# Performance work log

Measured on AMD Instinct MI355X. Metric: run time of the kernel, lower is better.

## Reference

```python
import jax, jax.numpy as jnp
import numpy as np

N_AUTHOR = 50000
N_PAPER = 50000
D_IN = 128      # input feature dim == hidden_channels so both layers share weight shapes
HID = 128
OUT = 32
N_LAYERS = 2
N_EDGES = 800000
NEG_SLOPE = 0.01  # F.leaky_relu default


def setup_inputs() -> dict:
    key = jax.random.key(0)
    ks = jax.random.split(key, 10)
    return {
        "x_author": jax.random.normal(ks[0], (N_AUTHOR, D_IN), jnp.float32),
        "x_paper": jax.random.normal(ks[1], (N_PAPER, D_IN), jnp.float32),
        # edge_index[0] = source node ids, edge_index[1] = destination node ids
        "edge_writes": jax.random.randint(ks[2], (2, N_EDGES), 0, N_PAPER, jnp.int32),      # author -> paper
        "edge_written_by": jax.random.randint(ks[3], (2, N_EDGES), 0, N_AUTHOR, jnp.int32),  # paper  -> author
        "edge_cites": jax.random.randint(ks[4], (2, N_EDGES), 0, N_PAPER, jnp.int32),        # paper  -> paper
        # SAGEConv params, stacked [layer, relation, in, out]; relation order:
        # 0: writes (a->p), 1: written_by (p->a), 2: cites (p->p)
        "Wl": jax.random.normal(ks[5], (N_LAYERS, 3, D_IN, HID), jnp.float32) * 0.05,  # lin_l (messages, has bias)
        "bl": jnp.zeros((N_LAYERS, 3, HID), jnp.float32),
        "Wr": jax.random.normal(ks[6], (N_LAYERS, 3, D_IN, HID), jnp.float32) * 0.05,  # lin_r (root, no bias)
        "lin_W": jax.random.normal(ks[7], (HID, OUT), jnp.float32) * 0.05,
        "lin_b": jnp.zeros((OUT,), jnp.float32),
    }


def _mean_aggr(x_src, edge, n_dst):
    # mean of source features over incoming edges per destination node; 0 for isolated nodes
    src, dst = edge[0], edge[1]
    s = jax.ops.segment_sum(x_src[src], dst, num_segments=n_dst)           # [n_dst, d]
    cnt = jax.ops.segment_sum(jnp.ones((dst.shape[0],), x_src.dtype), dst, num_segments=n_dst)
    return s / jnp.maximum(cnt, 1.0)[:, None]


def _sage(x_src, x_dst, edge, W_l, b_l, W_r):
    # PyG SAGEConv (mean aggr): lin_l(mean_j x_src[j]) + lin_r(x_dst)
    return _mean_aggr(x_src, edge, x_dst.shape[0]) @ W_l + b_l + x_dst @ W_r


def reference(x_author, x_paper, edge_writes, edge_written_by, edge_cites,
              Wl, bl, Wr, lin_W, lin_b):
    a, p = x_author, x_paper
    for l in range(N_LAYERS):
        # HeteroConv default aggr='sum' over edge types sharing a dst node type
        p_new = (_sage(a, p, edge_writes, Wl[l, 0], bl[l, 0], Wr[l, 0])
                 + _sage(p, p, edge_cites, Wl[l, 2], bl[l, 2], Wr[l, 2]))
        a_new = _sage(p, a, edge_written_by, Wl[l, 1], bl[l, 1], Wr[l, 1])
        a = jax.nn.leaky_relu(a_new, NEG_SLOPE)
        p = jax.nn.leaky_relu(p_new, NEG_SLOPE)
    return a @ lin_W + lin_b  # [N_AUTHOR, OUT]
```

## Files before the change

### kernel.cpp

```cpp
#include <hip/hip_runtime.h>

#define NA 50000
#define NP 50000
#define NE 800000
#define D 128
#define OUTD 32
#define NSEG 150000
#define DD (D * D)
#define NCH 196
#define NBK 588
#define CHE 4096
#define ZROW 50000

typedef float f32x4 __attribute__((ext_vector_type(4)));
typedef short s16x8 __attribute__((ext_vector_type(8)));

__device__ __forceinline__ ushort f2b(float f) {
    uint x = __float_as_uint(f);
    x += ((x >> 16) & 1u) + 0x7fffu;
    return (ushort)(x >> 16);
}


#define CVT_BLOCKS 12500
#define PREP_BLOCKS 466
#define HIST_BLOCKS NBK

__global__ __launch_bounds__(256) void front(
    const float* __restrict__ xa, const float* __restrict__ xp,
    ushort* __restrict__ oa, ushort* __restrict__ op,
    const float* __restrict__ Wl, const float* __restrict__ Wr,
    const float* __restrict__ linW, const float* __restrict__ bl,
    ushort* __restrict__ wt, float* __restrict__ bsum_p,
    ushort* __restrict__ p1b,
    const int* __restrict__ dw, const int* __restrict__ dc, const int* __restrict__ dwb,
    int* __restrict__ Hglob)
{
    __shared__ int hist[NCH];
    int b = blockIdx.x, t = threadIdx.x;
    if (b < CVT_BLOCKS) {
        int i = b * 256 + t;
        const int per = NA * D / 4;
        const float* src; ushort* dst; int li;
        if (i < per) { src = xa; dst = oa; li = i; }
        else { src = xp; dst = op; li = i - per; }
        float4 v = *(const float4*)&src[(size_t)li * 4];
        ushort4 o;
        o.x = f2b(v.x); o.y = f2b(v.y); o.z = f2b(v.z); o.w = f2b(v.w);
        *(ushort4*)&dst[(size_t)li * 4] = o;
    } else if (b < CVT_BLOCKS + PREP_BLOCKS) {
        int b2 = b - CVT_BLOCKS;
        if (b2 < 448) {
            int job = b2 >> 6;
            int idx = (b2 & 63) * 256 + t;
            int n = idx >> 7, k = idx & 127;
            const float* src;
            float add = 0.f;
            switch (job) {
                case 0: src = Wl + 0 * DD; break;
                case 1: src = Wl + 2 * DD; break;
                case 2: src = Wr + 0 * DD; add = Wr[2 * DD + k * D + n]; break;
                case 3: src = Wl + 1 * DD; break;
                case 4: src = Wr + 1 * DD; break;
                case 5: src = Wl + 4 * DD; break;
                default: src = Wr + 4 * DD; break;
            }
            wt[(size_t)job * DD + idx] = f2b(src[k * D + n] + add);
        } else if (b2 < 464) {
            int idx = (b2 - 448) * 256 + t;
            int n = idx >> 7, k = idx & 127;
            wt[(size_t)7 * DD + idx] = f2b(linW[k * OUTD + n]);
        } else if (b2 == 464) {
            if (t < D) bsum_p[t] = bl[t] + bl[2 * D + t];
        } else {
            if (t < 64)       ((uint*)(oa + (size_t)ZROW * D))[t] = 0;
            else if (t < 128) ((uint*)(op + (size_t)ZROW * D))[t - 64] = 0;
            else if (t < 192) ((uint*)(p1b + (size_t)ZROW * D))[t - 128] = 0;
        }
    } else {
        int hb = b - CVT_BLOCKS - PREP_BLOCKS;
        int r = hb / NCH, c = hb % NCH;
        const int* dp = (r == 0) ? dw : ((r == 1) ? dc : dwb);
        for (int i = t; i < NCH; i += 256) hist[i] = 0;
        __syncthreads();
        int base = c * CHE;
#pragma unroll
        for (int i = 0; i < 16; ++i) {
            int e = base + i * 256 + t;
            if (e < NE) atomicAdd(&hist[dp[e] >> 8], 1);
        }
        __syncthreads();
        for (int dg = t; dg < NCH; dg += 256)
            Hglob[(r * NCH + dg) * NCH + c] = hist[dg];
    }
}


__global__ __launch_bounds__(64) void scan_chunks(
    const int* __restrict__ Hglob, int* __restrict__ OFF, int* __restrict__ T)
{
    int gd = blockIdx.x, t = threadIdx.x;
    int carry = 0;
#pragma unroll
    for (int rnd = 0; rnd < 4; ++rnd) {
        int idx = rnd * 64 + t;
        int v = (idx < NCH) ? Hglob[gd * NCH + idx] : 0;
        int x = v;
#pragma unroll
        for (int off = 1; off < 64; off <<= 1) {
            int y = __shfl_up(x, off, 64);
            if (t >= off) x += y;
        }
        if (idx < NCH) OFF[gd * NCH + idx] = carry + x - v;
        carry += __shfl(x, 63, 64);
    }
    if (t == 0) T[gd] = carry;
}


__global__ __launch_bounds__(64) void scan_buckets(
    const int* __restrict__ T, int* __restrict__ B)
{
    int t = threadIdx.x, carry = 0;
#pragma unroll
    for (int rnd = 0; rnd < 10; ++rnd) {
        int idx = rnd * 64 + t;
        int v = (idx < NBK) ? T[idx] : 0;
        int x = v;
#pragma unroll
        for (int off = 1; off < 64; off <<= 1) {
            int y = __shfl_up(x, off, 64);
            if (t >= off) x += y;
        }
        if (idx < NBK) B[idx] = carry + x - v;
        carry += __shfl(x, 63, 64);
    }
}


__global__ __launch_bounds__(256) void bucket_scatter(
    const int* __restrict__ sw, const int* __restrict__ dw,
    const int* __restrict__ sc_, const int* __restrict__ dc,
    const int* __restrict__ swb, const int* __restrict__ dwb,
    const int* __restrict__ B, const int* __restrict__ OFF,
    uint* __restrict__ bucketed)
{
    __shared__ int lbase[NCH];
    __shared__ int cnt2[NCH];
    int b = blockIdx.x, t = threadIdx.x;
    int r = b / NCH, c = b % NCH;
    const int* sp = (r == 0) ? sw : ((r == 1) ? sc_ : swb);
    const int* dp = (r == 0) ? dw : ((r == 1) ? dc : dwb);
    for (int i = t; i < NCH; i += 256) {
        int gd = r * NCH + i;
        lbase[i] = B[gd] + OFF[gd * NCH + c];
        cnt2[i] = 0;
    }
    __syncthreads();
    int base = c * CHE;
#pragma unroll
    for (int i = 0; i < 16; ++i) {
        int e = base + i * 256 + t;
        if (e < NE) {
            int d = dp[e], s = sp[e];
            int dg = d >> 8;
            int rk = atomicAdd(&cnt2[dg], 1);
            bucketed[lbase[dg] + rk] = ((uint)d << 16) | (uint)s;
        }
    }
}


__global__ __launch_bounds__(256) void bucket_sort(
    const uint* __restrict__ bucketed, const int* __restrict__ B,
    const int* __restrict__ T, ushort* __restrict__ csr16,
    int* __restrict__ rowptr)
{
    __shared__ int h[256], bb[256], c3[256];
    int gd = blockIdx.x, t = threadIdx.x;
    int r = gd / NCH, hb = gd % NCH;
    int beg = B[gd], n = T[gd];
    h[t] = 0; c3[t] = 0;
    __syncthreads();
    for (int i = t; i < n; i += 256)
        atomicAdd(&h[(bucketed[beg + i] >> 16) & 255], 1);
    __syncthreads();
    if (t < 64) {
        int carry = 0;
#pragma unroll
        for (int rnd = 0; rnd < 4; ++rnd) {
            int idx = rnd * 64 + t;
            int v = h[idx], x = v;
#pragma unroll
            for (int off = 1; off < 64; off <<= 1) {
                int y = __shfl_up(x, off, 64);
                if (t >= off) x += y;
            }
            bb[idx] = carry + x - v;
            carry += __shfl(x, 63, 64);
        }
    }
    __syncthreads();
    {
        int dst = hb * 256 + t;
        if (dst < 50000) rowptr[r * 50000 + dst] = beg + bb[t];
    }
    for (int i = t; i < n; i += 256) {
        uint rec = bucketed[beg + i];
        int low = (rec >> 16) & 255;
        int rk = atomicAdd(&c3[low], 1);
        csr16[beg + bb[low] + rk] = (ushort)(rec & 0xffffu);
    }
    if (gd == NBK - 1 && t == 0) rowptr[NSEG] = 3 * NE;
}


#define DOT2(a, u, m) asm("v_dot2_f32_bf16 %0, %1, %2, %0" : "+v"(a) : "v"(u), "v"(m))

__device__ __forceinline__ void gather_node(
    const ushort* __restrict__ x, const ushort* __restrict__ bk, int n,
    int l, int g, int c, ushort* __restrict__ outp)
{
    float acc[8];
#pragma unroll
    for (int k = 0; k < 8; ++k) acc[k] = 0.f;
    const uint mlo = 0x00003f80u;
    const uint mhi = 0x3f800000u;
    const uint cb = (uint)c * 16;

    for (int base = 0; base < n; base += 64) {
        int rem = n - base;
        int m = rem > 64 ? 64 : rem;
        int idx = (l < m) ? (int)bk[base + l] : ZROW;
        int mceil = (m + 3) & ~3;
#pragma unroll 2
        for (int j = 0; j < mceil; j += 4) {
            int row = __shfl(idx, j + g, 64);
            uint4 u = *(const uint4*)((const char*)x + (((uint)row << 8) + cb));
            DOT2(acc[0], u.x, mlo); DOT2(acc[1], u.x, mhi);
            DOT2(acc[2], u.y, mlo); DOT2(acc[3], u.y, mhi);
            DOT2(acc[4], u.z, mlo); DOT2(acc[5], u.z, mhi);
            DOT2(acc[6], u.w, mlo); DOT2(acc[7], u.w, mhi);
        }
    }
#pragma unroll
    for (int k = 0; k < 8; ++k) {
        acc[k] += __shfl_xor(acc[k], 16, 64);
        acc[k] += __shfl_xor(acc[k], 32, 64);
    }
    if (g == 0) {
        float scl = (n > 0) ? 1.0f / (float)n : 0.f;
        uint4 o;
        o.x = (uint)f2b(acc[0] * scl) | ((uint)f2b(acc[1] * scl) << 16);
        o.y = (uint)f2b(acc[2] * scl) | ((uint)f2b(acc[3] * scl) << 16);
        o.z = (uint)f2b(acc[4] * scl) | ((uint)f2b(acc[5] * scl) << 16);
        o.w = (uint)f2b(acc[6] * scl) | ((uint)f2b(acc[7] * scl) << 16);
        *(uint4*)&outp[c * 8] = o;
    }
}

__global__ __launch_bounds__(256) void gather3(
    const ushort* __restrict__ xa, const ushort* __restrict__ xp,
    const int* __restrict__ rowptr, const ushort* __restrict__ csr16,
    ushort* __restrict__ agg3)
{
    int wid = (blockIdx.x * 256 + threadIdx.x) >> 6;
    if (wid >= NSEG) return;
    const ushort* x = (wid < 50000) ? xa : xp;
    int l = threadIdx.x & 63;
    int beg = __builtin_amdgcn_readfirstlane(rowptr[wid]);
    int end = __builtin_amdgcn_readfirstlane(rowptr[wid + 1]);
    gather_node(x, csr16 + beg, end - beg, l, l >> 4, l & 15,
                agg3 + (size_t)wid * D);
}

__global__ __launch_bounds__(256) void gather_l1(
    const ushort* __restrict__ x, const int* __restrict__ rowptr,
    const ushort* __restrict__ csr16, ushort* __restrict__ out)
{
    int wid = (blockIdx.x * 256 + threadIdx.x) >> 6;
    if (wid >= NA) return;
    int l = threadIdx.x & 63;
    int beg = __builtin_amdgcn_readfirstlane(rowptr[100000 + wid]);
    int end = __builtin_amdgcn_readfirstlane(rowptr[100000 + wid + 1]);
    gather_node(x, csr16 + beg, end - beg, l, l >> 4, l & 15,
                out + (size_t)wid * D);
}


#define LDA 136

__device__ __forceinline__ void gemm_core(
    ushort* As, f32x4 (&acc)[2][4],
    const ushort* __restrict__ A0, const ushort* __restrict__ WT0,
    const ushort* __restrict__ A1, const ushort* __restrict__ WT1,
    const ushort* __restrict__ A2, const ushort* __restrict__ WT2,
    int nseg, int brow, int M)
{
    const int t = threadIdx.x;
    const int w = t >> 6;
    const int l = t & 63;
    const int wr = w >> 1, wc = w & 1;
    const int l15 = l & 15, l4 = l >> 4;

    for (int s = 0; s < nseg; ++s) {
        const ushort* A = (s == 0) ? A0 : ((s == 1) ? A1 : A2);
        const ushort* WT = (s == 0) ? WT0 : ((s == 1) ? WT1 : WT2);

        if (s) __syncthreads();
#pragma unroll
        for (int it = 0; it < 4; ++it) {
            int f = it * 256 + t;
            int row = f >> 4, cc = f & 15;
            int grow = brow + row;
            float4 v = make_float4(0.f, 0.f, 0.f, 0.f);
            if (grow < M) v = *(const float4*)&A[(size_t)grow * D + cc * 8];
            *(float4*)&As[row * LDA + cc * 8] = v;
        }
        s16x8 Bf[4][4];
#pragma unroll
        for (int ni = 0; ni < 4; ++ni)
#pragma unroll
            for (int ks = 0; ks < 4; ++ks)
                Bf[ni][ks] = *(const s16x8*)&WT[(size_t)(wc * 64 + ni * 16 + l15) * D + ks * 32 + l4 * 8];
        __syncthreads();

#pragma unroll
        for (int ks = 0; ks < 4; ++ks) {
            s16x8 af[2];
#pragma unroll
            for (int mi = 0; mi < 2; ++mi)
                af[mi] = *(const s16x8*)&As[(wr * 32 + mi * 16 + l15) * LDA + ks * 32 + l4 * 8];
#pragma unroll
            for (int mi = 0; mi < 2; ++mi)
#pragma unroll
                for (int ni = 0; ni < 4; ++ni)
                    acc[mi][ni] = __builtin_amdgcn_mfma_f32_16x16x32_bf16(
                        af[mi], Bf[ni][ks], acc[mi][ni], 0, 0, 0);
        }
    }
}

__global__ __launch_bounds__(256) void gemm_pair(
    const ushort* __restrict__ agg3, const ushort* __restrict__ xb_p,
    const ushort* __restrict__ xb_a, const ushort* __restrict__ wt,
    const float* __restrict__ bsum_p, const float* __restrict__ bl,
    ushort* __restrict__ p1b, ushort* __restrict__ a1b)
{
    __shared__ ushort As[64 * LDA];
    const int t = threadIdx.x;
    const int w = t >> 6;
    const int l = t & 63;
    const int wr = w >> 1, wc = w & 1;
    const int l15 = l & 15, l4 = l >> 4;

    f32x4 acc[2][4];
#pragma unroll
    for (int i = 0; i < 2; ++i)
#pragma unroll
        for (int j = 0; j < 4; ++j) acc[i][j] = (f32x4){0.f, 0.f, 0.f, 0.f};

    bool isP = blockIdx.x < 782;
    int bIdx = isP ? blockIdx.x : blockIdx.x - 782;
    int brow = bIdx * 64;
    const float* bias;
    ushort* C;
    if (isP) {
        gemm_core(As, acc, agg3, wt + 0 * DD, agg3 + (size_t)50000 * D, wt + 1 * DD,
                  xb_p, wt + 2 * DD, 3, brow, NP);
        bias = bsum_p; C = p1b;
    } else {
        gemm_core(As, acc, agg3 + (size_t)100000 * D, wt + 3 * DD, xb_a, wt + 4 * DD,
                  nullptr, nullptr, 2, brow, NA);
        bias = bl + 1 * D; C = a1b;
    }

#pragma unroll
    for (int mi = 0; mi < 2; ++mi) {
#pragma unroll
        for (int ni = 0; ni < 4; ++ni) {
            int col = wc * 64 + ni * 16 + l15;
            float bb = bias[col];
#pragma unroll
            for (int r = 0; r < 4; ++r) {
                int grow = brow + wr * 32 + mi * 16 + l4 * 4 + r;
                if (grow >= 50000) continue;
                float v = acc[mi][ni][r] + bb;
                v = v > 0.f ? v : 0.01f * v;
                C[(size_t)grow * D + col] = f2b(v);
            }
        }
    }
}

__global__ __launch_bounds__(256) void gemm_final(
    const ushort* __restrict__ A0, const ushort* __restrict__ WT0,
    const ushort* __restrict__ A1, const ushort* __restrict__ WT1,
    const float* __restrict__ bias,
    const ushort* __restrict__ linWT, const float* __restrict__ linb,
    float* __restrict__ fout, int M)
{
    __shared__ ushort As[64 * LDA];
    const int t = threadIdx.x;
    const int w = t >> 6;
    const int l = t & 63;
    const int wr = w >> 1, wc = w & 1;
    const int l15 = l & 15, l4 = l >> 4;
    const int brow = blockIdx.x * 64;

    f32x4 acc[2][4];
#pragma unroll
    for (int i = 0; i < 2; ++i)
#pragma unroll
        for (int j = 0; j < 4; ++j) acc[i][j] = (f32x4){0.f, 0.f, 0.f, 0.f};

    gemm_core(As, acc, A0, WT0, A1, WT1, nullptr, nullptr, 2, brow, M);

    __syncthreads();
#pragma unroll
    for (int mi = 0; mi < 2; ++mi) {
#pragma unroll
        for (int ni = 0; ni < 4; ++ni) {
            int col = wc * 64 + ni * 16 + l15;
            float bb = bias[col];
#pragma unroll
            for (int r = 0; r < 4; ++r) {
                int row = wr * 32 + mi * 16 + l4 * 4 + r;
                float v = acc[mi][ni][r] + bb;
                v = v > 0.f ? v : 0.01f * v;
                As[row * LDA + col] = f2b(v);
            }
        }
    }
    __syncthreads();
    f32x4 a2c[2];
    a2c[0] = (f32x4){0.f, 0.f, 0.f, 0.f};
    a2c[1] = (f32x4){0.f, 0.f, 0.f, 0.f};
#pragma unroll
    for (int ks = 0; ks < 4; ++ks) {
        s16x8 af = *(const s16x8*)&As[(w * 16 + l15) * LDA + ks * 32 + l4 * 8];
#pragma unroll
        for (int ni = 0; ni < 2; ++ni) {
            s16x8 bf = *(const s16x8*)&linWT[(size_t)(ni * 16 + l15) * D + ks * 32 + l4 * 8];
            a2c[ni] = __builtin_amdgcn_mfma_f32_16x16x32_bf16(af, bf, a2c[ni], 0, 0, 0);
        }
    }
#pragma unroll
    for (int ni = 0; ni < 2; ++ni) {
        int col = ni * 16 + l15;
        float bb = linb[col];
#pragma unroll
        for (int r = 0; r < 4; ++r) {
            int grow = brow + w * 16 + l4 * 4 + r;
            if (grow < M) fout[(size_t)grow * OUTD + col] = a2c[ni][r] + bb;
        }
    }
}


extern "C" void kernel_launch(void* const* d_in, const int* in_sizes, int n_in,
                              void* d_out, int out_size, void* d_ws, size_t ws_size,
                              hipStream_t stream)
{
    const float* x_author = (const float*)d_in[0];
    const float* x_paper  = (const float*)d_in[1];
    const int*   e_w      = (const int*)d_in[2];
    const int*   e_wb     = (const int*)d_in[3];
    const int*   e_c      = (const int*)d_in[4];
    const float* Wl       = (const float*)d_in[5];
    const float* bl       = (const float*)d_in[6];
    const float* Wr       = (const float*)d_in[7];
    const float* linW     = (const float*)d_in[8];
    const float* linb     = (const float*)d_in[9];
    float* out = (float*)d_out;

    int* ib = (int*)d_ws;
    int* Hglob  = ib;
    int* OFF    = ib + 115248;
    int* T      = ib + 230496;
    int* B      = ib + 231084;
    int* rowptr = ib + 231680;
    uint* bucketed = (uint*)(ib + 381696);
    ushort* csr16  = (ushort*)(ib + 2781696);
    float* bsum_p  = (float*)(ib + 3981696);
    ushort* ub = (ushort*)(ib + 3981824);
    const size_t R1 = 50001 * (size_t)D;
    ushort* wt   = ub;
    ushort* xb_a = ub + 131072;
    ushort* xb_p = xb_a + R1;
    ushort* agg3 = xb_p + R1;
    ushort* p1b  = agg3 + (size_t)NSEG * D;
    ushort* a1b  = p1b + R1;
    ushort* g2b  = agg3;

    front<<<CVT_BLOCKS + PREP_BLOCKS + HIST_BLOCKS, 256, 0, stream>>>(
        x_author, x_paper, xb_a, xb_p,
        Wl, Wr, linW, bl, wt, bsum_p, p1b,
        e_w + NE, e_c + NE, e_wb + NE, Hglob);

    scan_chunks<<<NBK, 64, 0, stream>>>(Hglob, OFF, T);
    scan_buckets<<<1, 64, 0, stream>>>(T, B);

    bucket_scatter<<<NBK, 256, 0, stream>>>(
        e_w, e_w + NE, e_c, e_c + NE, e_wb, e_wb + NE, B, OFF, bucketed);

    bucket_sort<<<NBK, 256, 0, stream>>>(bucketed, B, T, csr16, rowptr);

    gather3<<<NSEG * 64 / 256, 256, 0, stream>>>(xb_a, xb_p, rowptr, csr16, agg3);

    gemm_pair<<<1564, 256, 0, stream>>>(agg3, xb_p, xb_a, wt, bsum_p, bl, p1b, a1b);

    gather_l1<<<NA * 64 / 256, 256, 0, stream>>>(p1b, rowptr, csr16, g2b);

    gemm_final<<<(NA + 63) / 64, 256, 0, stream>>>(
        g2b, wt + 5 * DD, a1b, wt + 6 * DD, bl + 4 * D, wt + 7 * DD, linb, out, NA);
}
```

Baseline: 247.4 us.

## Process four destination nodes per wavefront in gather kernels

Each wavefront now gathers neighbours for four destination nodes at once, interleaving their row loads so more independent memory requests are in flight per wave. Launch grids shrink by four accordingly, and lists longer than 64 entries fall back to a per-node tail loop. The trade-off is lanes wasted padding to the longest of the four lists, plus higher register use from the wider accumulators, which may lower occupancy.

Measured after the change: 255.3 us. +3.2%, slower.

```diff
diff --git a/kernel.cpp b/kernel.cpp
--- a/kernel.cpp
+++ b/kernel.cpp
@@ -217,45 +217,101 @@
 
 #define DOT2(a, u, m) asm("v_dot2_f32_bf16 %0, %1, %2, %0" : "+v"(a) : "v"(u), "v"(m))
 
-__device__ __forceinline__ void gather_node(
-    const ushort* __restrict__ x, const ushort* __restrict__ bk, int n,
-    int l, int g, int c, ushort* __restrict__ outp)
-{
-    float acc[8];
-#pragma unroll
-    for (int k = 0; k < 8; ++k) acc[k] = 0.f;
+__device__ __forceinline__ void gather4_core(
+    const ushort* __restrict__ x0, const ushort* __restrict__ x1, int thr,
+    const int* __restrict__ rowptr, int wid0,
+    const ushort* __restrict__ csr16, ushort* __restrict__ out)
+{
+    const int l = threadIdx.x & 63;
+    const int g = l >> 4, c = l & 15;
+    const uint cb = (uint)c * 16;
     const uint mlo = 0x00003f80u;
     const uint mhi = 0x3f800000u;
-    const uint cb = (uint)c * 16;
-
-    for (int base = 0; base < n; base += 64) {
-        int rem = n - base;
-        int m = rem > 64 ? 64 : rem;
-        int idx = (l < m) ? (int)bk[base + l] : ZROW;
-        int mceil = (m + 3) & ~3;
-#pragma unroll 2
-        for (int j = 0; j < mceil; j += 4) {
-            int row = __shfl(idx, j + g, 64);
-            uint4 u = *(const uint4*)((const char*)x + (((uint)row << 8) + cb));
-            DOT2(acc[0], u.x, mlo); DOT2(acc[1], u.x, mhi);
-            DOT2(acc[2], u.y, mlo); DOT2(acc[3], u.y, mhi);
-            DOT2(acc[4], u.z, mlo); DOT2(acc[5], u.z, mhi);
-            DOT2(acc[6], u.w, mlo); DOT2(acc[7], u.w, mhi);
-        }
-    }
-#pragma unroll
-    for (int k = 0; k < 8; ++k) {
-        acc[k] += __shfl_xor(acc[k], 16, 64);
-        acc[k] += __shfl_xor(acc[k], 32, 64);
-    }
-    if (g == 0) {
-        float scl = (n > 0) ? 1.0f / (float)n : 0.f;
-        uint4 o;
-        o.x = (uint)f2b(acc[0] * scl) | ((uint)f2b(acc[1] * scl) << 16);
-        o.y = (uint)f2b(acc[2] * scl) | ((uint)f2b(acc[3] * scl) << 16);
-        o.z = (uint)f2b(acc[4] * scl) | ((uint)f2b(acc[5] * scl) << 16);
-        o.w = (uint)f2b(acc[6] * scl) | ((uint)f2b(acc[7] * scl) << 16);
-        *(uint4*)&outp[c * 8] = o;
+
+    int rp = rowptr[wid0 + (l > 4 ? 4 : l)];
+    int beg[4], n[4], mc[4];
+#pragma unroll
+    for (int k = 0; k < 4; ++k) {
+        beg[k] = __builtin_amdgcn_readfirstlane(__shfl(rp, k, 64));
+        int e = __builtin_amdgcn_readfirstlane(__shfl(rp, k + 1, 64));
+        n[k] = e - beg[k];
+        int m = n[k] > 64 ? 64 : n[k];
+        mc[k] = (m + 3) & ~3;
+    }
+    int maxmc = mc[0];
+    maxmc = mc[1] > maxmc ? mc[1] : maxmc;
+    maxmc = mc[2] > maxmc ? mc[2] : maxmc;
+    maxmc = mc[3] > maxmc ? mc[3] : maxmc;
+
+    const ushort* xs[4];
+#pragma unroll
+    for (int k = 0; k < 4; ++k) xs[k] = (wid0 + k < thr) ? x0 : x1;
+
+    int idx[4];
+#pragma unroll
+    for (int k = 0; k < 4; ++k) {
+        int m = n[k] > 64 ? 64 : n[k];
+        idx[k] = (l < m) ? (int)csr16[beg[k] + l] : ZROW;
+    }
+
+    float acc[4][8];
+#pragma unroll
+    for (int k = 0; k < 4; ++k)
+#pragma unroll
+        for (int i = 0; i < 8; ++i) acc[k][i] = 0.f;
+
+    for (int j = 0; j < maxmc; j += 4) {
+        uint4 u[4];
+#pragma unroll
+        for (int k = 0; k < 4; ++k) {
+            int row = __shfl(idx[k], j + g, 64);
+            u[k] = *(const uint4*)((const char*)xs[k] + (((uint)row << 8) + cb));
+        }
+#pragma unroll
+        for (int k = 0; k < 4; ++k) {
+            DOT2(acc[k][0], u[k].x, mlo); DOT2(acc[k][1], u[k].x, mhi);
+            DOT2(acc[k][2], u[k].y, mlo); DOT2(acc[k][3], u[k].y, mhi);
+            DOT2(acc[k][4], u[k].z, mlo); DOT2(acc[k][5], u[k].z, mhi);
+            DOT2(acc[k][6], u[k].w, mlo); DOT2(acc[k][7], u[k].w, mhi);
+        }
+    }
+
+#pragma unroll
+    for (int k = 0; k < 4; ++k) {
+        if (n[k] > 64) {
+            for (int base = 64; base < n[k]; base += 64) {
+                int rem = n[k] - base;
+                int m = rem > 64 ? 64 : rem;
+                int id2 = (l < m) ? (int)csr16[beg[k] + base + l] : ZROW;
+                int mc2 = (m + 3) & ~3;
+                for (int j = 0; j < mc2; j += 4) {
+                    int row = __shfl(id2, j + g, 64);
+                    uint4 u = *(const uint4*)((const char*)xs[k] + (((uint)row << 8) + cb));
+                    DOT2(acc[k][0], u.x, mlo); DOT2(acc[k][1], u.x, mhi);
+                    DOT2(acc[k][2], u.y, mlo); DOT2(acc[k][3], u.y, mhi);
+                    DOT2(acc[k][4], u.z, mlo); DOT2(acc[k][5], u.z, mhi);
+                    DOT2(acc[k][6], u.w, mlo); DOT2(acc[k][7], u.w, mhi);
+                }
+            }
+        }
+    }
+
+#pragma unroll
+    for (int k = 0; k < 4; ++k) {
+#pragma unroll
+        for (int i = 0; i < 8; ++i) {
+            acc[k][i] += __shfl_xor(acc[k][i], 16, 64);
+            acc[k][i] += __shfl_xor(acc[k][i], 32, 64);
+        }
+        if (g == 0) {
+            float scl = (n[k] > 0) ? 1.0f / (float)n[k] : 0.f;
+            uint4 o;
+            o.x = (uint)f2b(acc[k][0] * scl) | ((uint)f2b(acc[k][1] * scl) << 16);
+            o.y = (uint)f2b(acc[k][2] * scl) | ((uint)f2b(acc[k][3] * scl) << 16);
+            o.z = (uint)f2b(acc[k][4] * scl) | ((uint)f2b(acc[k][5] * scl) << 16);
+            o.w = (uint)f2b(acc[k][6] * scl) | ((uint)f2b(acc[k][7] * scl) << 16);
+            *(uint4*)&out[(size_t)(wid0 + k) * D + c * 8] = o;
+        }
     }
 }
 
@@ -264,27 +320,20 @@
     const int* __restrict__ rowptr, const ushort* __restrict__ csr16,
     ushort* __restrict__ agg3)
 {
-    int wid = (blockIdx.x * 256 + threadIdx.x) >> 6;
-    if (wid >= NSEG) return;
-    const ushort* x = (wid < 50000) ? xa : xp;
-    int l = threadIdx.x & 63;
-    int beg = __builtin_amdgcn_readfirstlane(rowptr[wid]);
-    int end = __builtin_amdgcn_readfirstlane(rowptr[wid + 1]);
-    gather_node(x, csr16 + beg, end - beg, l, l >> 4, l & 15,
-                agg3 + (size_t)wid * D);
+    int wv = (blockIdx.x * 256 + threadIdx.x) >> 6;
+    int wid0 = wv * 4;
+    if (wid0 >= NSEG) return;
+    gather4_core(xa, xp, 50000, rowptr, wid0, csr16, agg3);
 }
 
 __global__ __launch_bounds__(256) void gather_l1(
     const ushort* __restrict__ x, const int* __restrict__ rowptr,
     const ushort* __restrict__ csr16, ushort* __restrict__ out)
 {
-    int wid = (blockIdx.x * 256 + threadIdx.x) >> 6;
-    if (wid >= NA) return;
-    int l = threadIdx.x & 63;
-    int beg = __builtin_amdgcn_readfirstlane(rowptr[100000 + wid]);
-    int end = __builtin_amdgcn_readfirstlane(rowptr[100000 + wid + 1]);
-    gather_node(x, csr16 + beg, end - beg, l, l >> 4, l & 15,
-                out + (size_t)wid * D);
+    int wv = (blockIdx.x * 256 + threadIdx.x) >> 6;
+    int wid0 = wv * 4;
+    if (wid0 >= NA) return;
+    gather4_core(x, x, NSEG, rowptr + 100000, wid0, csr16, out);
 }
 
 
@@ -506,11 +555,11 @@
 
     bucket_sort<<<NBK, 256, 0, stream>>>(bucketed, B, T, csr16, rowptr);
 
-    gather3<<<NSEG * 64 / 256, 256, 0, stream>>>(xb_a, xb_p, rowptr, csr16, agg3);
+    gather3<<<NSEG / 4 / 4, 256, 0, stream>>>(xb_a, xb_p, rowptr, csr16, agg3);
 
     gemm_pair<<<1564, 256, 0, stream>>>(agg3, xb_p, xb_a, wt, bsum_p, bl, p1b, a1b);
 
-    gather_l1<<<NA * 64 / 256, 256, 0, stream>>>(p1b, rowptr, csr16, g2b);
+    gather_l1<<<NA / 4 / 4, 256, 0, stream>>>(p1b, rowptr, csr16, g2b);
 
     gemm_final<<<(NA + 63) / 64, 256, 0, stream>>>(
         g2b, wt + 5 * DD, a1b, wt + 6 * DD, bl + 4 * D, wt + 7 * DD, linb, out, NA);
```

## Fuse neighbor mean-aggregation gathers into the SAGE GEMM kernels via LDS staging

Applied to the files above, without the earlier changes.

The separate gather kernels, which wrote bf16 aggregates to global memory, are removed. The GEMM blocks now gather their own 64 destination rows straight into shared memory and run MFMA on them. This drops the global round trip for agg3/g2b and two kernel launches. Weight fragments are now loaded per k-step instead of being preloaded into registers. Occupancy falls from 2344 gather blocks to 1564/782 fused blocks, and the GEMM blocks now stall on irregular gathers, so latency hiding may suffer.

After: 294.9 us. 1.19x slower.

```diff
diff --git a/kernel.cpp b/kernel.cpp
--- a/kernel.cpp
+++ b/kernel.cpp
@@ -215,144 +215,110 @@
 }
 
 
+#define LDA 136
 #define DOT2(a, u, m) asm("v_dot2_f32_bf16 %0, %1, %2, %0" : "+v"(a) : "v"(u), "v"(m))
 
-__device__ __forceinline__ void gather_node(
-    const ushort* __restrict__ x, const ushort* __restrict__ bk, int n,
-    int l, int g, int c, ushort* __restrict__ outp)
-{
-    float acc[8];
-#pragma unroll
-    for (int k = 0; k < 8; ++k) acc[k] = 0.f;
+__device__ __forceinline__ void gather_seg(
+    const ushort* __restrict__ x, const int* __restrict__ rowptr,
+    int gnbase, const ushort* __restrict__ csr16, ushort* As)
+{
+    const int t = threadIdx.x;
+    const int w = t >> 6, l = t & 63;
+    const int g = l >> 4, c = l & 15;
+    const uint cb = (uint)c * 16;
     const uint mlo = 0x00003f80u;
     const uint mhi = 0x3f800000u;
-    const uint cb = (uint)c * 16;
-
-    for (int base = 0; base < n; base += 64) {
-        int rem = n - base;
-        int m = rem > 64 ? 64 : rem;
-        int idx = (l < m) ? (int)bk[base + l] : ZROW;
-        int mceil = (m + 3) & ~3;
 #pragma unroll 2
-        for (int j = 0; j < mceil; j += 4) {
-            int row = __shfl(idx, j + g, 64);
-            uint4 u = *(const uint4*)((const char*)x + (((uint)row << 8) + cb));
-            DOT2(acc[0], u.x, mlo); DOT2(acc[1], u.x, mhi);
-            DOT2(acc[2], u.y, mlo); DOT2(acc[3], u.y, mhi);
-            DOT2(acc[4], u.z, mlo); DOT2(acc[5], u.z, mhi);
-            DOT2(acc[6], u.w, mlo); DOT2(acc[7], u.w, mhi);
-        }
-    }
-#pragma unroll
-    for (int k = 0; k < 8; ++k) {
-        acc[k] += __shfl_xor(acc[k], 16, 64);
-        acc[k] += __shfl_xor(acc[k], 32, 64);
-    }
-    if (g == 0) {
-        float scl = (n > 0) ? 1.0f / (float)n : 0.f;
-        uint4 o;
-        o.x = (uint)f2b(acc[0] * scl) | ((uint)f2b(acc[1] * scl) << 16);
-        o.y = (uint)f2b(acc[2] * scl) | ((uint)f2b(acc[3] * scl) << 16);
-        o.z = (uint)f2b(acc[4] * scl) | ((uint)f2b(acc[5] * scl) << 16);
-        o.w = (uint)f2b(acc[6] * scl) | ((uint)f2b(acc[7] * scl) << 16);
-        *(uint4*)&outp[c * 8] = o;
-    }
-}
-
-__global__ __launch_bounds__(256) void gather3(
-    const ushort* __restrict__ xa, const ushort* __restrict__ xp,
+    for (int i = 0; i < 16; ++i) {
+        int nl = w * 16 + i;
+        int gn = gnbase + nl;
+        gn = gn > NSEG - 1 ? NSEG - 1 : gn;
+        int beg = __builtin_amdgcn_readfirstlane(rowptr[gn]);
+        int end = __builtin_amdgcn_readfirstlane(rowptr[gn + 1]);
+        int n = end - beg;
+        float acc[8];
+#pragma unroll
+        for (int k2 = 0; k2 < 8; ++k2) acc[k2] = 0.f;
+        for (int base = 0; base < n; base += 64) {
+            int rem = n - base;
+            int m = rem > 64 ? 64 : rem;
+            int idx = (l < m) ? (int)csr16[beg + base + l] : ZROW;
+            int mceil = (m + 3) & ~3;
+#pragma unroll 2
+            for (int j = 0; j < mceil; j += 4) {
+                int row = __shfl(idx, j + g, 64);
+                uint4 u = *(const uint4*)((const char*)x + (((uint)row << 8) + cb));
+                DOT2(acc[0], u.x, mlo); DOT2(acc[1], u.x, mhi);
+                DOT2(acc[2], u.y, mlo); DOT2(acc[3], u.y, mhi);
+                DOT2(acc[4], u.z, mlo); DOT2(acc[5], u.z, mhi);
+                DOT2(acc[6], u.w, mlo); DOT2(acc[7], u.w, mhi);
+            }
+        }
+#pragma unroll
+        for (int k2 = 0; k2 < 8; ++k2) {
+            acc[k2] += __shfl_xor(acc[k2], 16, 64);
+            acc[k2] += __shfl_xor(acc[k2], 32, 64);
+        }
+        if (g == 0) {
+            float scl = (n > 0) ? 1.0f / (float)n : 0.f;
+            uint4 o;
+            o.x = (uint)f2b(acc[0] * scl) | ((uint)f2b(acc[1] * scl) << 16);
+            o.y = (uint)f2b(acc[2] * scl) | ((uint)f2b(acc[3] * scl) << 16);
+            o.z = (uint)f2b(acc[4] * scl) | ((uint)f2b(acc[5] * scl) << 16);
+            o.w = (uint)f2b(acc[6] * scl) | ((uint)f2b(acc[7] * scl) << 16);
+            *(uint4*)&As[nl * LDA + c * 8] = o;
+        }
+    }
+}
+
+__device__ __forceinline__ void stage_direct(
+    const ushort* __restrict__ A, int brow, int M, ushort* As)
+{
+    const int t = threadIdx.x;
+#pragma unroll
+    for (int it = 0; it < 4; ++it) {
+        int f = it * 256 + t;
+        int row = f >> 4, cc = f & 15;
+        int grow = brow + row;
+        float4 v = make_float4(0.f, 0.f, 0.f, 0.f);
+        if (grow < M) v = *(const float4*)&A[(size_t)grow * D + cc * 8];
+        *(float4*)&As[row * LDA + cc * 8] = v;
+    }
+}
+
+__device__ __forceinline__ void mfma_seg(
+    const ushort* __restrict__ As, const ushort* __restrict__ WT,
+    f32x4 (&acc)[2][4])
+{
+    const int t = threadIdx.x, w = t >> 6, l = t & 63;
+    const int wr = w >> 1, wc = w & 1, l15 = l & 15, l4 = l >> 4;
+#pragma unroll
+    for (int ks = 0; ks < 4; ++ks) {
+        s16x8 af[2];
+#pragma unroll
+        for (int mi = 0; mi < 2; ++mi)
+            af[mi] = *(const s16x8*)&As[(wr * 32 + mi * 16 + l15) * LDA + ks * 32 + l4 * 8];
+#pragma unroll
+        for (int ni = 0; ni < 4; ++ni) {
+            s16x8 bf = *(const s16x8*)&WT[(size_t)(wc * 64 + ni * 16 + l15) * D + ks * 32 + l4 * 8];
+#pragma unroll
+            for (int mi = 0; mi < 2; ++mi)
+                acc[mi][ni] = __builtin_amdgcn_mfma_f32_16x16x32_bf16(af[mi], bf, acc[mi][ni], 0, 0, 0);
+        }
+    }
+}
+
+__global__ __launch_bounds__(256) void fused_pair(
+    const ushort* __restrict__ xb_a, const ushort* __restrict__ xb_p,
     const int* __restrict__ rowptr, const ushort* __restrict__ csr16,
-    ushort* __restrict__ agg3)
-{
-    int wid = (blockIdx.x * 256 + threadIdx.x) >> 6;
-    if (wid >= NSEG) return;
-    const ushort* x = (wid < 50000) ? xa : xp;
-    int l = threadIdx.x & 63;
-    int beg = __builtin_amdgcn_readfirstlane(rowptr[wid]);
-    int end = __builtin_amdgcn_readfirstlane(rowptr[wid + 1]);
-    gather_node(x, csr16 + beg, end - beg, l, l >> 4, l & 15,
-                agg3 + (size_t)wid * D);
-}
-
-__global__ __launch_bounds__(256) void gather_l1(
-    const ushort* __restrict__ x, const int* __restrict__ rowptr,
-    const ushort* __restrict__ csr16, ushort* __restrict__ out)
-{
-    int wid = (blockIdx.x * 256 + threadIdx.x) >> 6;
-    if (wid >= NA) return;
-    int l = threadIdx.x & 63;
-    int beg = __builtin_amdgcn_readfirstlane(rowptr[100000 + wid]);
-    int end = __builtin_amdgcn_readfirstlane(rowptr[100000 + wid + 1]);
-    gather_node(x, csr16 + beg, end - beg, l, l >> 4, l & 15,
-                out + (size_t)wid * D);
-}
-
-
-#define LDA 136
-
-__device__ __forceinline__ void gemm_core(
-    ushort* As, f32x4 (&acc)[2][4],
-    const ushort* __restrict__ A0, const ushort* __restrict__ WT0,
-    const ushort* __restrict__ A1, const ushort* __restrict__ WT1,
-    const ushort* __restrict__ A2, const ushort* __restrict__ WT2,
-    int nseg, int brow, int M)
-{
-    const int t = threadIdx.x;
-    const int w = t >> 6;
-    const int l = t & 63;
-    const int wr = w >> 1, wc = w & 1;
-    const int l15 = l & 15, l4 = l >> 4;
-
-    for (int s = 0; s < nseg; ++s) {
-        const ushort* A = (s == 0) ? A0 : ((s == 1) ? A1 : A2);
-        const ushort* WT = (s == 0) ? WT0 : ((s == 1) ? WT1 : WT2);
-
-        if (s) __syncthreads();
-#pragma unroll
-        for (int it = 0; it < 4; ++it) {
-            int f = it * 256 + t;
-            int row = f >> 4, cc = f & 15;
-            int grow = brow + row;
-            float4 v = make_float4(0.f, 0.f, 0.f, 0.f);
-            if (grow < M) v = *(const float4*)&A[(size_t)grow * D + cc * 8];
-            *(float4*)&As[row * LDA + cc * 8] = v;
-        }
-        s16x8 Bf[4][4];
-#pragma unroll
-        for (int ni = 0; ni < 4; ++ni)
-#pragma unroll
-            for (int ks = 0; ks < 4; ++ks)
-                Bf[ni][ks] = *(const s16x8*)&WT[(size_t)(wc * 64 + ni * 16 + l15) * D + ks * 32 + l4 * 8];
-        __syncthreads();
-
-#pragma unroll
-        for (int ks = 0; ks < 4; ++ks) {
-            s16x8 af[2];
-#pragma unroll
-            for (int mi = 0; mi < 2; ++mi)
-                af[mi] = *(const s16x8*)&As[(wr * 32 + mi * 16 + l15) * LDA + ks * 32 + l4 * 8];
-#pragma unroll
-            for (int mi = 0; mi < 2; ++mi)
-#pragma unroll
-                for (int ni = 0; ni < 4; ++ni)
-                    acc[mi][ni] = __builtin_amdgcn_mfma_f32_16x16x32_bf16(
-                        af[mi], Bf[ni][ks], acc[mi][ni], 0, 0, 0);
-        }
-    }
-}
-
-__global__ __launch_bounds__(256) void gemm_pair(
-    const ushort* __restrict__ agg3, const ushort* __restrict__ xb_p,
-    const ushort* __restrict__ xb_a, const ushort* __restrict__ wt,
-    const float* __restrict__ bsum_p, const float* __restrict__ bl,
+    const ushort* __restrict__ wt, const float* __restrict__ bsum_p,
+    const float* __restrict__ bl,
     ushort* __restrict__ p1b, ushort* __restrict__ a1b)
 {
     __shared__ ushort As[64 * LDA];
     const int t = threadIdx.x;
-    const int w = t >> 6;
-    const int l = t & 63;
-    const int wr = w >> 1, wc = w & 1;
-    const int l15 = l & 15, l4 = l >> 4;
+    const int w = t >> 6, l = t & 63;
+    const int wr = w >> 1, wc = w & 1, l15 = l & 15, l4 = l >> 4;
 
     f32x4 acc[2][4];
 #pragma unroll
@@ -361,20 +327,32 @@
         for (int j = 0; j < 4; ++j) acc[i][j] = (f32x4){0.f, 0.f, 0.f, 0.f};
 
     bool isP = blockIdx.x < 782;
-    int bIdx = isP ? blockIdx.x : blockIdx.x - 782;
-    int brow = bIdx * 64;
-    const float* bias;
-    ushort* C;
+    int brow = (isP ? blockIdx.x : blockIdx.x - 782) * 64;
+
     if (isP) {
-        gemm_core(As, acc, agg3, wt + 0 * DD, agg3 + (size_t)50000 * D, wt + 1 * DD,
-                  xb_p, wt + 2 * DD, 3, brow, NP);
-        bias = bsum_p; C = p1b;
+        gather_seg(xb_a, rowptr, 0 + brow, csr16, As);
+        __syncthreads();
+        mfma_seg(As, wt + 0 * DD, acc);
+        __syncthreads();
+        gather_seg(xb_p, rowptr, 50000 + brow, csr16, As);
+        __syncthreads();
+        mfma_seg(As, wt + 1 * DD, acc);
+        __syncthreads();
+        stage_direct(xb_p, brow, NP, As);
+        __syncthreads();
+        mfma_seg(As, wt + 2 * DD, acc);
     } else {
-        gemm_core(As, acc, agg3 + (size_t)100000 * D, wt + 3 * DD, xb_a, wt + 4 * DD,
-                  nullptr, nullptr, 2, brow, NA);
-        bias = bl + 1 * D; C = a1b;
-    }
-
+        gather_seg(xb_p, rowptr, 100000 + brow, csr16, As);
+        __syncthreads();
+        mfma_seg(As, wt + 3 * DD, acc);
+        __syncthreads();
+        stage_direct(xb_a, brow, NA, As);
+        __syncthreads();
+        mfma_seg(As, wt + 4 * DD, acc);
+    }
+
+    const float* bias = isP ? bsum_p : (bl + 1 * D);
+    ushort* C = isP ? p1b : a1b;
 #pragma unroll
     for (int mi = 0; mi < 2; ++mi) {
 #pragma unroll
@@ -393,19 +371,17 @@
     }
 }
 
-__global__ __launch_bounds__(256) void gemm_final(
-    const ushort* __restrict__ A0, const ushort* __restrict__ WT0,
-    const ushort* __restrict__ A1, const ushort* __restrict__ WT1,
-    const float* __restrict__ bias,
+__global__ __launch_bounds__(256) void fused_final(
+    const ushort* __restrict__ p1b, const ushort* __restrict__ a1b,
+    const int* __restrict__ rowptr, const ushort* __restrict__ csr16,
+    const ushort* __restrict__ wt, const float* __restrict__ bl,
     const ushort* __restrict__ linWT, const float* __restrict__ linb,
-    float* __restrict__ fout, int M)
+    float* __restrict__ fout)
 {
     __shared__ ushort As[64 * LDA];
     const int t = threadIdx.x;
-    const int w = t >> 6;
-    const int l = t & 63;
-    const int wr = w >> 1, wc = w & 1;
-    const int l15 = l & 15, l4 = l >> 4;
+    const int w = t >> 6, l = t & 63;
+    const int wr = w >> 1, wc = w & 1, l15 = l & 15, l4 = l >> 4;
     const int brow = blockIdx.x * 64;
 
     f32x4 acc[2][4];
@@ -414,9 +390,16 @@
 #pragma unroll
         for (int j = 0; j < 4; ++j) acc[i][j] = (f32x4){0.f, 0.f, 0.f, 0.f};
 
-    gemm_core(As, acc, A0, WT0, A1, WT1, nullptr, nullptr, 2, brow, M);
-
-    __syncthreads();
+    gather_seg(p1b, rowptr, 100000 + brow, csr16, As);
+    __syncthreads();
+    mfma_seg(As, wt + 5 * DD, acc);
+    __syncthreads();
+    stage_direct(a1b, brow, NA, As);
+    __syncthreads();
+    mfma_seg(As, wt + 6 * DD, acc);
+
+    __syncthreads();
+    const float* bias = bl + 4 * D;
 #pragma unroll
     for (int mi = 0; mi < 2; ++mi) {
 #pragma unroll
@@ -452,7 +435,7 @@
 #pragma unroll
         for (int r = 0; r < 4; ++r) {
             int grow = brow + w * 16 + l4 * 4 + r;
-            if (grow < M) fout[(size_t)grow * OUTD + col] = a2c[ni][r] + bb;
+            if (grow < NA) fout[(size_t)grow * OUTD + col] = a2c[ni][r] + bb;
         }
     }
 }
@@ -488,10 +471,8 @@
     ushort* wt   = ub;
     ushort* xb_a = ub + 131072;
     ushort* xb_p = xb_a + R1;
-    ushort* agg3 = xb_p + R1;
-    ushort* p1b  = agg3 + (size_t)NSEG * D;
+    ushort* p1b  = xb_p + R1;
     ushort* a1b  = p1b + R1;
-    ushort* g2b  = agg3;
 
     front<<<CVT_BLOCKS + PREP_BLOCKS + HIST_BLOCKS, 256, 0, stream>>>(
         x_author, x_paper, xb_a, xb_p,
@@ -506,12 +487,9 @@
 
     bucket_sort<<<NBK, 256, 0, stream>>>(bucketed, B, T, csr16, rowptr);
 
-    gather3<<<NSEG * 64 / 256, 256, 0, stream>>>(xb_a, xb_p, rowptr, csr16, agg3);
-
-    gemm_pair<<<1564, 256, 0, stream>>>(agg3, xb_p, xb_a, wt, bsum_p, bl, p1b, a1b);
-
-    gather_l1<<<NA * 64 / 256, 256, 0, stream>>>(p1b, rowptr, csr16, g2b);
-
-    gemm_final<<<(NA + 63) / 64, 256, 0, stream>>>(
-        g2b, wt + 5 * DD, a1b, wt + 6 * DD, bl + 4 * D, wt + 7 * DD, linb, out, NA);
-}
+    fused_pair<<<1564, 256, 0, stream>>>(
+        xb_a, xb_p, rowptr, csr16, wt, bsum_p, bl, p1b, a1b);
+
+    fused_final<<<782, 256, 0, stream>>>(
+        p1b, a1b, rowptr, csr16, wt, bl, wt + 7 * DD, linb, out);
+}
```

## Replace scan-based bucket offsets with fixed-capacity buckets and atomic cursors

Applied to the files above, without the earlier changes.

Edge bucketing no longer builds a global histogram and prefix scan. Each destination bucket now gets a fixed capacity (CAP2) region, and the per-chunk scatter happens inside the front kernel using an atomic cursor per bucket, with records staged in shared memory. This removes three kernel launches (scan_chunks, scan_buckets, bucket_scatter) and a second read of the edge arrays. Because buckets are no longer contiguous, per-node counts are stored separately for the gathers, and the gather loop unroll is raised from 2 to 4. The risk is bucket overflow if any bucket exceeds 4608 edges; that holds for the uniform random test inputs but is not guaranteed in general.

After: 248.4 us. Within noise of the previous version (+0.4%).

```diff
diff --git a/kernel.cpp b/kernel.cpp
--- a/kernel.cpp
+++ b/kernel.cpp
@@ -10,6 +10,7 @@
 #define NCH 196
 #define NBK 588
 #define CHE 4096
+#define CAP2 4608
 #define ZROW 50000
 
 typedef float f32x4 __attribute__((ext_vector_type(4)));
@@ -24,19 +25,22 @@
 
 #define CVT_BLOCKS 12500
 #define PREP_BLOCKS 466
-#define HIST_BLOCKS NBK
-
-__global__ __launch_bounds__(256) void front(
+#define SCAT_BLOCKS NBK
+
+__global__ __launch_bounds__(256) void front2(
     const float* __restrict__ xa, const float* __restrict__ xp,
     ushort* __restrict__ oa, ushort* __restrict__ op,
     const float* __restrict__ Wl, const float* __restrict__ Wr,
     const float* __restrict__ linW, const float* __restrict__ bl,
     ushort* __restrict__ wt, float* __restrict__ bsum_p,
     ushort* __restrict__ p1b,
-    const int* __restrict__ dw, const int* __restrict__ dc, const int* __restrict__ dwb,
-    int* __restrict__ Hglob)
-{
-    __shared__ int hist[NCH];
+    const int* __restrict__ sw, const int* __restrict__ dw,
+    const int* __restrict__ sc_, const int* __restrict__ dc,
+    const int* __restrict__ swb, const int* __restrict__ dwb,
+    int* __restrict__ cursor, uint* __restrict__ bucketed)
+{
+    __shared__ uint recbuf[CHE];
+    __shared__ int hist[NCH], gbase[NCH], cnt2[NCH];
     int b = blockIdx.x, t = threadIdx.x;
     if (b < CVT_BLOCKS) {
         int i = b * 256 + t;
@@ -80,106 +84,48 @@
     } else {
         int hb = b - CVT_BLOCKS - PREP_BLOCKS;
         int r = hb / NCH, c = hb % NCH;
+        const int* sp = (r == 0) ? sw : ((r == 1) ? sc_ : swb);
         const int* dp = (r == 0) ? dw : ((r == 1) ? dc : dwb);
-        for (int i = t; i < NCH; i += 256) hist[i] = 0;
+        for (int i = t; i < NCH; i += 256) { hist[i] = 0; cnt2[i] = 0; }
         __syncthreads();
         int base = c * CHE;
 #pragma unroll
         for (int i = 0; i < 16; ++i) {
             int e = base + i * 256 + t;
-            if (e < NE) atomicAdd(&hist[dp[e] >> 8], 1);
+            uint rec = 0xFFFFFFFFu;
+            if (e < NE) {
+                int d = dp[e], s = sp[e];
+                rec = ((uint)d << 16) | (uint)s;
+                atomicAdd(&hist[d >> 8], 1);
+            }
+            recbuf[i * 256 + t] = rec;
         }
         __syncthreads();
-        for (int dg = t; dg < NCH; dg += 256)
-            Hglob[(r * NCH + dg) * NCH + c] = hist[dg];
-    }
-}
-
-
-__global__ __launch_bounds__(64) void scan_chunks(
-    const int* __restrict__ Hglob, int* __restrict__ OFF, int* __restrict__ T)
-{
-    int gd = blockIdx.x, t = threadIdx.x;
-    int carry = 0;
-#pragma unroll
-    for (int rnd = 0; rnd < 4; ++rnd) {
-        int idx = rnd * 64 + t;
-        int v = (idx < NCH) ? Hglob[gd * NCH + idx] : 0;
-        int x = v;
-#pragma unroll
-        for (int off = 1; off < 64; off <<= 1) {
-            int y = __shfl_up(x, off, 64);
-            if (t >= off) x += y;
-        }
-        if (idx < NCH) OFF[gd * NCH + idx] = carry + x - v;
-        carry += __shfl(x, 63, 64);
-    }
-    if (t == 0) T[gd] = carry;
-}
-
-
-__global__ __launch_bounds__(64) void scan_buckets(
-    const int* __restrict__ T, int* __restrict__ B)
-{
-    int t = threadIdx.x, carry = 0;
-#pragma unroll
-    for (int rnd = 0; rnd < 10; ++rnd) {
-        int idx = rnd * 64 + t;
-        int v = (idx < NBK) ? T[idx] : 0;
-        int x = v;
-#pragma unroll
-        for (int off = 1; off < 64; off <<= 1) {
-            int y = __shfl_up(x, off, 64);
-            if (t >= off) x += y;
-        }
-        if (idx < NBK) B[idx] = carry + x - v;
-        carry += __shfl(x, 63, 64);
-    }
-}
-
-
-__global__ __launch_bounds__(256) void bucket_scatter(
-    const int* __restrict__ sw, const int* __restrict__ dw,
-    const int* __restrict__ sc_, const int* __restrict__ dc,
-    const int* __restrict__ swb, const int* __restrict__ dwb,
-    const int* __restrict__ B, const int* __restrict__ OFF,
-    uint* __restrict__ bucketed)
-{
-    __shared__ int lbase[NCH];
-    __shared__ int cnt2[NCH];
-    int b = blockIdx.x, t = threadIdx.x;
-    int r = b / NCH, c = b % NCH;
-    const int* sp = (r == 0) ? sw : ((r == 1) ? sc_ : swb);
-    const int* dp = (r == 0) ? dw : ((r == 1) ? dc : dwb);
-    for (int i = t; i < NCH; i += 256) {
-        int gd = r * NCH + i;
-        lbase[i] = B[gd] + OFF[gd * NCH + c];
-        cnt2[i] = 0;
-    }
-    __syncthreads();
-    int base = c * CHE;
-#pragma unroll
-    for (int i = 0; i < 16; ++i) {
-        int e = base + i * 256 + t;
-        if (e < NE) {
-            int d = dp[e], s = sp[e];
-            int dg = d >> 8;
-            int rk = atomicAdd(&cnt2[dg], 1);
-            bucketed[lbase[dg] + rk] = ((uint)d << 16) | (uint)s;
-        }
-    }
-}
-
-
-__global__ __launch_bounds__(256) void bucket_sort(
-    const uint* __restrict__ bucketed, const int* __restrict__ B,
-    const int* __restrict__ T, ushort* __restrict__ csr16,
-    int* __restrict__ rowptr)
+        for (int i = t; i < NCH; i += 256)
+            gbase[i] = (r * NCH + i) * CAP2 + atomicAdd(&cursor[r * NCH + i], hist[i]);
+        __syncthreads();
+#pragma unroll
+        for (int i = 0; i < 16; ++i) {
+            uint rec = recbuf[i * 256 + t];
+            if (rec != 0xFFFFFFFFu) {
+                int dg = rec >> 24;
+                int rk = atomicAdd(&cnt2[dg], 1);
+                bucketed[gbase[dg] + rk] = rec;
+            }
+        }
+    }
+}
+
+
+__global__ __launch_bounds__(256) void bucket_sort2(
+    const uint* __restrict__ bucketed, const int* __restrict__ cursor,
+    ushort* __restrict__ csr16, int* __restrict__ rowptr, int* __restrict__ cntd)
 {
     __shared__ int h[256], bb[256], c3[256];
     int gd = blockIdx.x, t = threadIdx.x;
     int r = gd / NCH, hb = gd % NCH;
-    int beg = B[gd], n = T[gd];
+    int beg = gd * CAP2;
+    int n = cursor[gd];
     h[t] = 0; c3[t] = 0;
     __syncthreads();
     for (int i = t; i < n; i += 256)
@@ -203,7 +149,10 @@
     __syncthreads();
     {
         int dst = hb * 256 + t;
-        if (dst < 50000) rowptr[r * 50000 + dst] = beg + bb[t];
+        if (dst < 50000) {
+            rowptr[r * 50000 + dst] = beg + bb[t];
+            cntd[r * 50000 + dst] = h[t];
+        }
     }
     for (int i = t; i < n; i += 256) {
         uint rec = bucketed[beg + i];
@@ -211,7 +160,6 @@
         int rk = atomicAdd(&c3[low], 1);
         csr16[beg + bb[low] + rk] = (ushort)(rec & 0xffffu);
     }
-    if (gd == NBK - 1 && t == 0) rowptr[NSEG] = 3 * NE;
 }
 
 
@@ -233,7 +181,7 @@
         int m = rem > 64 ? 64 : rem;
         int idx = (l < m) ? (int)bk[base + l] : ZROW;
         int mceil = (m + 3) & ~3;
-#pragma unroll 2
+#pragma unroll 4
         for (int j = 0; j < mceil; j += 4) {
             int row = __shfl(idx, j + g, 64);
             uint4 u = *(const uint4*)((const char*)x + (((uint)row << 8) + cb));
@@ -261,29 +209,30 @@
 
 __global__ __launch_bounds__(256) void gather3(
     const ushort* __restrict__ xa, const ushort* __restrict__ xp,
-    const int* __restrict__ rowptr, const ushort* __restrict__ csr16,
-    ushort* __restrict__ agg3)
+    const int* __restrict__ rowptr, const int* __restrict__ cntd,
+    const ushort* __restrict__ csr16, ushort* __restrict__ agg3)
 {
     int wid = (blockIdx.x * 256 + threadIdx.x) >> 6;
     if (wid >= NSEG) return;
     const ushort* x = (wid < 50000) ? xa : xp;
     int l = threadIdx.x & 63;
     int beg = __builtin_amdgcn_readfirstlane(rowptr[wid]);
-    int end = __builtin_amdgcn_readfirstlane(rowptr[wid + 1]);
-    gather_node(x, csr16 + beg, end - beg, l, l >> 4, l & 15,
+    int n = __builtin_amdgcn_readfirstlane(cntd[wid]);
+    gather_node(x, csr16 + beg, n, l, l >> 4, l & 15,
                 agg3 + (size_t)wid * D);
 }
 
 __global__ __launch_bounds__(256) void gather_l1(
     const ushort* __restrict__ x, const int* __restrict__ rowptr,
-    const ushort* __restrict__ csr16, ushort* __restrict__ out)
+    const int* __restrict__ cntd, const ushort* __restrict__ csr16,
+    ushort* __restrict__ out)
 {
     int wid = (blockIdx.x * 256 + threadIdx.x) >> 6;
     if (wid >= NA) return;
     int l = threadIdx.x & 63;
     int beg = __builtin_amdgcn_readfirstlane(rowptr[100000 + wid]);
-    int end = __builtin_amdgcn_readfirstlane(rowptr[100000 + wid + 1]);
-    gather_node(x, csr16 + beg, end - beg, l, l >> 4, l & 15,
+    int n = __builtin_amdgcn_readfirstlane(cntd[100000 + wid]);
+    gather_node(x, csr16 + beg, n, l, l >> 4, l & 15,
                 out + (size_t)wid * D);
 }
 
@@ -475,15 +424,13 @@
     float* out = (float*)d_out;
 
     int* ib = (int*)d_ws;
-    int* Hglob  = ib;
-    int* OFF    = ib + 115248;
-    int* T      = ib + 230496;
-    int* B      = ib + 231084;
-    int* rowptr = ib + 231680;
-    uint* bucketed = (uint*)(ib + 381696);
-    ushort* csr16  = (ushort*)(ib + 2781696);
-    float* bsum_p  = (float*)(ib + 3981696);
-    ushort* ub = (ushort*)(ib + 3981824);
+    int* cursor  = ib;
+    int* rowptr  = ib + 640;
+    int* cntd    = ib + 150656;
+    uint* bucketed = (uint*)(ib + 300672);
+    ushort* csr16  = (ushort*)(ib + 3010176);
+    float* bsum_p  = (float*)(ib + 4364928);
+    ushort* ub = (ushort*)(ib + 4365056);
     const size_t R1 = 50001 * (size_t)D;
     ushort* wt   = ub;
     ushort* xb_a = ub + 131072;
@@ -493,24 +440,21 @@
     ushort* a1b  = p1b + R1;
     ushort* g2b  = agg3;
 
-    front<<<CVT_BLOCKS + PREP_BLOCKS + HIST_BLOCKS, 256, 0, stream>>>(
+    hipMemsetAsync(cursor, 0, NBK * sizeof(int), stream);
+
+    front2<<<CVT_BLOCKS + PREP_BLOCKS + SCAT_BLOCKS, 256, 0, stream>>>(
         x_author, x_paper, xb_a, xb_p,
         Wl, Wr, linW, bl, wt, bsum_p, p1b,
-        e_w + NE, e_c + NE, e_wb + NE, Hglob);
-
-    scan_chunks<<<NBK, 64, 0, stream>>>(Hglob, OFF, T);
-    scan_buckets<<<1, 64, 0, stream>>>(T, B);
-
-    bucket_scatter<<<NBK, 256, 0, stream>>>(
-        e_w, e_w + NE, e_c, e_c + NE, e_wb, e_wb + NE, B, OFF, bucketed);
-
-    bucket_sort<<<NBK, 256, 0, stream>>>(bucketed, B, T, csr16, rowptr);
-
-    gather3<<<NSEG * 64 / 256, 256, 0, stream>>>(xb_a, xb_p, rowptr, csr16, agg3);
+        e_w, e_w + NE, e_c, e_c + NE, e_wb, e_wb + NE,
+        cursor, bucketed);
+
+    bucket_sort2<<<NBK, 256, 0, stream>>>(bucketed, cursor, csr16, rowptr, cntd);
+
+    gather3<<<NSEG * 64 / 256, 256, 0, stream>>>(xb_a, xb_p, rowptr, cntd, csr16, agg3);
 
     gemm_pair<<<1564, 256, 0, stream>>>(agg3, xb_p, xb_a, wt, bsum_p, bl, p1b, a1b);
 
-    gather_l1<<<NA * 64 / 256, 256, 0, stream>>>(p1b, rowptr, csr16, g2b);
+    gather_l1<<<NA * 64 / 256, 256, 0, stream>>>(p1b, rowptr, cntd, csr16, g2b);
 
     gemm_final<<<(NA + 63) / 64, 256, 0, stream>>>(
         g2b, wt + 5 * DD, a1b, wt + 6 * DD, bl + 4 * D, wt + 7 * DD, linb, out, NA);
```
